# Optimization experiments

Hardware: AMD Instinct MI355X
Metric: run time of the kernel (lower is better)

The kernel has to match this reference:

```python
import jax, jax.numpy as jnp
import numpy as np

B, N, D, H = 2, 4096, 768, 12
HD = D // H  # head_dim = 64


def setup_inputs() -> dict:
    key = jax.random.key(0)
    k1, k2, k3, k4 = jax.random.split(key, 4)
    s = 1.0 / np.sqrt(D)
    return {
        "x": jax.random.normal(k1, (B, N, D), dtype=jnp.float32),
        "W_kqv": jax.random.normal(k2, (H, D, 3 * HD), dtype=jnp.float32) * s,
        "W_proj": jax.random.normal(k3, (D, D), dtype=jnp.float32) * s,
        "b_proj": jax.random.normal(k4, (D,), dtype=jnp.float32) * 0.02,
    }


def reference(x, W_kqv, W_proj, b_proj):
    # Per-head fused KQV projection: [B,N,D] x [H,D,3*HD] -> [B,H,N,3*HD]
    kqv = jnp.einsum("bnd,hde->bhne", x, W_kqv)
    # split order in source: k, q, v
    k, q, v = jnp.split(kqv, 3, axis=-1)  # each [B,H,N,HD]
    scale = 1.0 / np.sqrt(HD)
    scores = jnp.einsum("bhqd,bhkd->bhqk", q, k) * scale  # [B,H,N,N]
    causal = jnp.tril(jnp.ones((N, N), dtype=bool))
    scores = jnp.where(causal, scores, -jnp.inf)
    probs = jax.nn.softmax(scores, axis=-1)
    out = jnp.einsum("bhqk,bhkd->bhqd", probs, v)  # [B,H,N,HD]
    # concat heads along feature dim -> [B,N,D]
    out = out.transpose(0, 2, 1, 3).reshape(B, N, D)
    # output projection (dropout_rate=0.0 -> identity)
    return out @ W_proj.T + b_proj
```

## Files before the change

### kernel.cpp

```cpp
#include <hip/hip_runtime.h>

typedef _Float16 half8 __attribute__((ext_vector_type(8)));
typedef __fp16 fp16x2 __attribute__((ext_vector_type(2)));
typedef float floatx4 __attribute__((ext_vector_type(4)));
typedef float floatx16 __attribute__((ext_vector_type(16)));

#define MFMA_F16(a, b, c) __builtin_amdgcn_mfma_f32_16x16x32_f16((a), (b), (c), 0, 0, 0)
#define MFMA32(a, b, c) __builtin_amdgcn_mfma_f32_32x32x16_f16((a), (b), (c), 0, 0, 0)

__device__ __forceinline__ unsigned short f2h_bits(float f) {
    union { _Float16 h; unsigned short u; } cv;
    cv.h = (_Float16)f;
    return cv.u;
}

__device__ __forceinline__ float exp2_hw(float x) {
#if __has_builtin(__builtin_amdgcn_exp2f)
    return __builtin_amdgcn_exp2f(x);
#else
    return exp2f(x);
#endif
}

__device__ __forceinline__ unsigned pkrtz(float a, float b) {
    union { fp16x2 h; unsigned u; } cv;
    cv.h = __builtin_amdgcn_cvt_pkrtz(a, b);
    return cv.u;
}

__device__ __forceinline__ void swap32(unsigned a, unsigned b, int hi32,
                                       unsigned& r0, unsigned& r1) {
#if __has_builtin(__builtin_amdgcn_permlane32_swap)
    auto r = __builtin_amdgcn_permlane32_swap((int)a, (int)b, false, false);
    r0 = (unsigned)r[0];
    r1 = (unsigned)r[1];
#else
    unsigned ax = (unsigned)__shfl_xor((int)a, 32, 64);
    unsigned bx = (unsigned)__shfl_xor((int)b, 32, 64);
    r0 = hi32 ? bx : a;
    r1 = hi32 ? b : ax;
#endif
}

__device__ __forceinline__ float xhalf_max(float x) {
#if __has_builtin(__builtin_amdgcn_permlane32_swap)
    auto r = __builtin_amdgcn_permlane32_swap(__float_as_int(x), __float_as_int(x), false, false);
    return fmaxf(__int_as_float(r[0]), __int_as_float(r[1]));
#else
    return fmaxf(x, __shfl_xor(x, 32, 64));
#endif
}
__device__ __forceinline__ float xhalf_add(float x) {
#if __has_builtin(__builtin_amdgcn_permlane32_swap)
    auto r = __builtin_amdgcn_permlane32_swap(__float_as_int(x), __float_as_int(x), false, false);
    return __int_as_float(r[0]) + __int_as_float(r[1]);
#else
    return x + __shfl_xor(x, 32, 64);
#endif
}

__device__ __forceinline__ float bperm_f(int srclane, float v) {
    return __int_as_float(__builtin_amdgcn_ds_bpermute(srclane << 2, __float_as_int(v)));
}

__global__ void conv_x_kernel(const float* __restrict__ x, unsigned short* __restrict__ xb) {
    int i = blockIdx.x * 256 + threadIdx.x;
    float4 v = ((const float4*)x)[i];
    ushort4 o;
    o.x = f2h_bits(v.x); o.y = f2h_bits(v.y); o.z = f2h_bits(v.z); o.w = f2h_bits(v.w);
    ((ushort4*)xb)[i] = o;
}

__global__ void conv_wkqv_kernel(const float* __restrict__ w, unsigned short* __restrict__ wT) {
    int t = blockIdx.x * 256 + threadIdx.x;
    int d = t % 768;
    int hc = t / 768;
    int h = hc / 192;
    int c = hc - h * 192;
    float v = w[(h * 768 + d) * 192 + c];
    if (c >= 64 && c < 128) v *= 0.18033688011112042f;
    wT[t] = f2h_bits(v);
}

__global__ void conv_wproj_kernel(const float* __restrict__ w, unsigned short* __restrict__ wb) {
    int i = blockIdx.x * 256 + threadIdx.x;
    float4 v = ((const float4*)w)[i];
    ushort4 o;
    o.x = f2h_bits(v.x); o.y = f2h_bits(v.y); o.z = f2h_bits(v.z); o.w = f2h_bits(v.w);
    ((ushort4*)wb)[i] = o;
}

template <int EPI>
__global__ __launch_bounds__(256, 2) void gemm_bt_kernel(
    const unsigned short* __restrict__ A, const unsigned short* __restrict__ Bt,
    unsigned short* __restrict__ o_q, unsigned short* __restrict__ o_k,
    unsigned short* __restrict__ o_vt, float* __restrict__ o_f32,
    const float* __restrict__ bias, int Ntiles) {
    __shared__ unsigned short sA[128 * 64];
    __shared__ unsigned short sB[128 * 64];
    const int tid = threadIdx.x;
    const int lo = tid & 15;
    const int hi = (tid >> 4) & 3;
    const int wid = tid >> 6;
    const int wr = wid >> 1;
    const int wc = wid & 1;
    const int bm = blockIdx.x / Ntiles;
    const int bn = blockIdx.x % Ntiles;
    const size_t rowA0 = (size_t)bm * 128;
    const size_t rowB0 = (size_t)bn * 128;

    const floatx4 ZERO = {0.f, 0.f, 0.f, 0.f};
    floatx4 acc[4][4];
#pragma unroll
    for (int i = 0; i < 4; ++i)
#pragma unroll
        for (int j = 0; j < 4; ++j) acc[i][j] = ZERO;

    const int ldsWaveBase = (tid & 0xC0) << 3;

    for (int kt = 0; kt < 768; kt += 64) {
        __syncthreads();
#pragma unroll
        for (int it = 0; it < 4; ++it) {
            int g = it * 256 + tid;
            int row = g >> 3;
            int slot = g & 7;
            int koff = kt + ((slot ^ (row & 7)) << 3);
            const unsigned short* srcA = A + (rowA0 + row) * 768 + koff;
            const unsigned short* srcB = Bt + (rowB0 + row) * 768 + koff;
            unsigned short* dA = &sA[it * 2048 + ldsWaveBase];
            unsigned short* dB = &sB[it * 2048 + ldsWaveBase];
            __builtin_amdgcn_global_load_lds(
                (const __attribute__((address_space(1))) unsigned int*)srcA,
                (__attribute__((address_space(3))) unsigned int*)dA, 16, 0, 0);
            __builtin_amdgcn_global_load_lds(
                (const __attribute__((address_space(1))) unsigned int*)srcB,
                (__attribute__((address_space(3))) unsigned int*)dB, 16, 0, 0);
        }
        __syncthreads();
#pragma unroll
        for (int kc = 0; kc < 2; ++kc) {
            half8 av[4], bv[4];
#pragma unroll
            for (int mi = 0; mi < 4; ++mi) {
                int row = wr * 64 + mi * 16 + lo;
                av[mi] = *(const half8*)&sA[row * 64 + (((kc * 4 + hi) ^ (lo & 7)) << 3)];
            }
#pragma unroll
            for (int ni = 0; ni < 4; ++ni) {
                int row = wc * 64 + ni * 16 + lo;
                bv[ni] = *(const half8*)&sB[row * 64 + (((kc * 4 + hi) ^ (lo & 7)) << 3)];
            }
#pragma unroll
            for (int mi = 0; mi < 4; ++mi)
#pragma unroll
                for (int ni = 0; ni < 4; ++ni)
                    acc[mi][ni] = MFMA_F16(av[mi], bv[ni], acc[mi][ni]);
        }
    }

    if (EPI == 0) {
#pragma unroll
        for (int ni = 0; ni < 4; ++ni) {
            int gn = (int)rowB0 + wc * 64 + ni * 16 + lo;
            unsigned h = (unsigned)gn / 192u;
            int c = gn - (int)h * 192;
#pragma unroll
            for (int mi = 0; mi < 4; ++mi) {
#pragma unroll
                for (int r = 0; r < 4; ++r) {
                    int gm = (int)rowA0 + wr * 64 + mi * 16 + hi * 4 + r;
                    int b = gm >> 12;
                    int n = gm & 4095;
                    int bh = b * 12 + (int)h;
                    unsigned short val = f2h_bits(acc[mi][ni][r]);
                    if (c < 64) {
                        int t = n >> 5;
                        size_t idx = ((((size_t)bh * 128 + t) * 4 + (c >> 4)) * 64 +
                                      (((c >> 3) & 1) * 32 + (n & 31))) * 8 + (c & 7);
                        o_k[idx] = val;
                    } else if (c < 128) {
                        int d = c - 64;
                        int t = n >> 5;
                        size_t idx = ((((size_t)bh * 128 + t) * 4 + (d >> 4)) * 64 +
                                      (((d >> 3) & 1) * 32 + (n & 31))) * 8 + (d & 7);
                        o_q[idx] = val;
                    } else {
                        int dv = c - 128;
                        int t = n >> 5;
                        int kin = n & 31;
                        size_t idx = ((((size_t)bh * 128 + t) * 4 +
                                       ((dv >> 5) * 2 + (kin >> 4))) * 64 +
                                      (((kin >> 3) & 1) * 32 + (dv & 31))) * 8 + (kin & 7);
                        o_vt[idx] = val;
                    }
                }
            }
        }
    } else {
#pragma unroll
        for (int mi = 0; mi < 4; ++mi)
#pragma unroll
            for (int ni = 0; ni < 4; ++ni) {
                int gn = (int)rowB0 + wc * 64 + ni * 16 + lo;
                float bs = bias[gn];
#pragma unroll
                for (int r = 0; r < 4; ++r) {
                    int gm = (int)rowA0 + wr * 64 + mi * 16 + hi * 4 + r;
                    o_f32[(size_t)gm * 768 + gn] = acc[mi][ni][r] + bs;
                }
            }
    }
}

__global__ __launch_bounds__(128, 3) void attn_kernel(
    const unsigned short* __restrict__ Qw, const unsigned short* __restrict__ Kw,
    const unsigned short* __restrict__ Vtw, unsigned short* __restrict__ Ow) {
    __shared__ float sM[64 * 35];
    const int tid = threadIdx.x;
    const int lane = tid & 63;
    const int wid = tid >> 6;
    const int l31 = lane & 31;
    const int hi32 = lane >> 5;
    const int bh = blockIdx.x % 24;
    const int band = 127 - blockIdx.x / 24;
    const int b = bh / 12;
    const int h = bh - b * 12;

    const unsigned short* QF = Qw + (size_t)bh * 262144;
    const unsigned short* KF = Kw + (size_t)bh * 262144;
    const unsigned short* VF = Vtw + (size_t)bh * 262144;

    const floatx16 Z16 = {0.f,0.f,0.f,0.f,0.f,0.f,0.f,0.f,0.f,0.f,0.f,0.f,0.f,0.f,0.f,0.f};

    const int q0 = band << 5;
    const int myq = q0 + l31;
    const int nk = (band >> 1) + 1;

    half8 qf[4];
#pragma unroll
    for (int ds = 0; ds < 4; ++ds)
        qf[ds] = *(const half8*)&QF[(((size_t)band * 4 + ds) * 64 + lane) * 8];

    floatx16 accO0 = Z16, accO1 = Z16;
    float mI = -1e30f, lI = 0.f;

    for (int i = wid; i < nk; i += 2) {
        const int kt = i << 6;
        const unsigned short* kb = &KF[(size_t)(2 * i) * 2048 + lane * 8];
        half8 kfa[4], kfb[4];
#pragma unroll
        for (int ds = 0; ds < 4; ++ds) {
            kfa[ds] = *(const half8*)(kb + ds * 512);
            kfb[ds] = *(const half8*)(kb + 2048 + ds * 512);
        }
        const unsigned short* vb0 = &VF[(size_t)(2 * i) * 2048 + lane * 8];
        half8 vf0[2][2], vf1[2][2];
#pragma unroll
        for (int dt = 0; dt < 2; ++dt)
#pragma unroll
            for (int j = 0; j < 2; ++j) {
                vf0[dt][j] = *(const half8*)(vb0 + (dt * 2 + j) * 512);
                vf1[dt][j] = *(const half8*)(vb0 + 2048 + (dt * 2 + j) * 512);
            }

        floatx16 s0 = Z16, s1 = Z16;
        __builtin_amdgcn_s_setprio(1);
#pragma unroll
        for (int ds = 0; ds < 4; ++ds) s0 = MFMA32(kfa[ds], qf[ds], s0);
#pragma unroll
        for (int ds = 0; ds < 4; ++ds) s1 = MFMA32(kfb[ds], qf[ds], s1);
        __builtin_amdgcn_s_setprio(0);

        if (i == nk - 1) {
#pragma unroll
            for (int r = 0; r < 16; ++r) {
                int crow = (r & 3) + ((r >> 2) << 3) + (hi32 << 2);
                if (kt + crow > myq) s0[r] = -1e30f;
                if (kt + 32 + crow > myq) s1[r] = -1e30f;
            }
        }

        float ma[8];
#pragma unroll
        for (int r = 0; r < 8; ++r)
            ma[r] = fmaxf(fmaxf(s0[2 * r], s0[2 * r + 1]),
                          fmaxf(s1[2 * r], s1[2 * r + 1]));
        float mx = fmaxf(fmaxf(fmaxf(ma[0], ma[1]), fmaxf(ma[2], ma[3])),
                         fmaxf(fmaxf(ma[4], ma[5]), fmaxf(ma[6], ma[7])));
        mx = xhalf_max(mx);

        if (!__all(mx <= mI + 8.0f)) {
            float mn = fmaxf(mI, mx);
            float sc = exp2_hw(mI - mn);
            mI = mn;
            lI *= sc;
#pragma unroll
            for (int r = 0; r < 16; ++r) {
                int src = (r & 3) + ((r >> 2) << 3) + (hi32 << 2);
                float scb = bperm_f(src, sc);
                accO0[r] *= scb;
                accO1[r] *= scb;
            }
        }

#pragma unroll
        for (int r = 0; r < 16; ++r) {
            s0[r] = exp2_hw(s0[r] - mI);
            s1[r] = exp2_hw(s1[r] - mI);
        }
        float sa[8];
#pragma unroll
        for (int r = 0; r < 8; ++r)
            sa[r] = (s0[2 * r] + s0[2 * r + 1]) + (s1[2 * r] + s1[2 * r + 1]);
        float ps = ((sa[0] + sa[1]) + (sa[2] + sa[3])) +
                   ((sa[4] + sa[5]) + (sa[6] + sa[7]));
        lI += xhalf_add(ps);

        {
            unsigned pA0 = pkrtz(s0[0], s0[1]),   pA1 = pkrtz(s0[2], s0[3]);
            unsigned pB0 = pkrtz(s0[4], s0[5]),   pB1 = pkrtz(s0[6], s0[7]);
            unsigned pC0 = pkrtz(s0[8], s0[9]),   pC1 = pkrtz(s0[10], s0[11]);
            unsigned pD0 = pkrtz(s0[12], s0[13]), pD1 = pkrtz(s0[14], s0[15]);
            unsigned w0, w1, w2, w3, u0, u1, u2, u3;
            swap32(pA0, pB0, hi32, w0, w2);
            swap32(pA1, pB1, hi32, w1, w3);
            swap32(pC0, pD0, hi32, u0, u2);
            swap32(pC1, pD1, hi32, u1, u3);
            union { unsigned u[4]; half8 h; } f0, f1;
            f0.u[0] = w0; f0.u[1] = w1; f0.u[2] = w2; f0.u[3] = w3;
            f1.u[0] = u0; f1.u[1] = u1; f1.u[2] = u2; f1.u[3] = u3;
            __builtin_amdgcn_s_setprio(1);
            accO0 = MFMA32(f0.h, vf0[0][0], accO0);
            accO0 = MFMA32(f1.h, vf0[0][1], accO0);
            accO1 = MFMA32(f0.h, vf0[1][0], accO1);
            accO1 = MFMA32(f1.h, vf0[1][1], accO1);
            __builtin_amdgcn_s_setprio(0);
        }
        {
            unsigned pA0 = pkrtz(s1[0], s1[1]),   pA1 = pkrtz(s1[2], s1[3]);
            unsigned pB0 = pkrtz(s1[4], s1[5]),   pB1 = pkrtz(s1[6], s1[7]);
            unsigned pC0 = pkrtz(s1[8], s1[9]),   pC1 = pkrtz(s1[10], s1[11]);
            unsigned pD0 = pkrtz(s1[12], s1[13]), pD1 = pkrtz(s1[14], s1[15]);
            unsigned w0, w1, w2, w3, u0, u1, u2, u3;
            swap32(pA0, pB0, hi32, w0, w2);
            swap32(pA1, pB1, hi32, w1, w3);
            swap32(pC0, pD0, hi32, u0, u2);
            swap32(pC1, pD1, hi32, u1, u3);
            union { unsigned u[4]; half8 h; } f0, f1;
            f0.u[0] = w0; f0.u[1] = w1; f0.u[2] = w2; f0.u[3] = w3;
            f1.u[0] = u0; f1.u[1] = u1; f1.u[2] = u2; f1.u[3] = u3;
            __builtin_amdgcn_s_setprio(1);
            accO0 = MFMA32(f0.h, vf1[0][0], accO0);
            accO0 = MFMA32(f1.h, vf1[0][1], accO0);
            accO1 = MFMA32(f0.h, vf1[1][0], accO1);
            accO1 = MFMA32(f1.h, vf1[1][1], accO1);
            __builtin_amdgcn_s_setprio(0);
        }
    }

    if (wid == 1) {
        float* dst = &sM[lane * 35];
        dst[0] = mI;
        dst[1] = lI;
#pragma unroll
        for (int r = 0; r < 16; ++r) { dst[2 + r] = accO0[r]; dst[18 + r] = accO1[r]; }
    }
    __syncthreads();
    if (wid == 0) {
        const float* src = &sM[lane * 35];
        float m1 = src[0], l1 = src[1];
        float mstar = fmaxf(mI, m1);
        float sc0 = exp2_hw(mI - mstar);
        float sc1 = exp2_hw(m1 - mstar);
        float lt = lI * sc0 + l1 * sc1;
        float inv = 1.0f / lt;
        float f0 = sc0 * inv, f1 = sc1 * inv;
#pragma unroll
        for (int r = 0; r < 16; ++r) {
            int crow = (r & 3) + ((r >> 2) << 3) + (hi32 << 2);
            float fb0 = bperm_f(crow, f0);
            float fb1 = bperm_f(crow, f1);
            float o0 = accO0[r] * fb0 + src[2 + r] * fb1;
            float o1 = accO1[r] * fb0 + src[18 + r] * fb1;
            int qrow = q0 + crow;
            size_t base = ((size_t)(b * 4096 + qrow)) * 768 + h * 64;
            Ow[base + l31] = f2h_bits(o0);
            Ow[base + 32 + l31] = f2h_bits(o1);
        }
    }
}

extern "C" void kernel_launch(void* const* d_in, const int* in_sizes, int n_in,
                              void* d_out, int out_size, void* d_ws, size_t ws_size,
                              hipStream_t stream) {
    const float* x = (const float*)d_in[0];
    const float* wkqv = (const float*)d_in[1];
    const float* wproj = (const float*)d_in[2];
    const float* bproj = (const float*)d_in[3];
    float* out = (float*)d_out;

    char* ws = (char*)d_ws;
    unsigned short* xb = (unsigned short*)(ws);
    unsigned short* wkqvT = (unsigned short*)(ws + 12582912);
    unsigned short* wprojB = (unsigned short*)(ws + 16121856);
    unsigned short* Qw = (unsigned short*)(ws + 17301504);
    unsigned short* Kw = (unsigned short*)(ws + 29884416);
    unsigned short* Vtw = (unsigned short*)(ws + 42467328);
    unsigned short* Ow = xb;
    if (ws_size < 55050240) return;

    conv_x_kernel<<<6144, 256, 0, stream>>>(x, xb);
    conv_wkqv_kernel<<<6912, 256, 0, stream>>>(wkqv, wkqvT);
    conv_wproj_kernel<<<576, 256, 0, stream>>>(wproj, wprojB);
    gemm_bt_kernel<0><<<64 * 18, 256, 0, stream>>>(xb, wkqvT, Qw, Kw, Vtw, nullptr, nullptr, 18);
    attn_kernel<<<24 * 128, 128, 0, stream>>>(Qw, Kw, Vtw, Ow);
    gemm_bt_kernel<1><<<64 * 6, 256, 0, stream>>>(Ow, wprojB, nullptr, nullptr, nullptr, out, bproj, 6);
}
```

Before: 162.9 us.

## Share K tiles across two query bands via double-buffered LDS in attention

Attention blocks now own two adjacent 32-row query bands, one per wave, instead of splitting one band's key range across the two waves. Each key tile is loaded once into double-buffered LDS with async global-to-LDS loads and read by both waves, which removes the cross-wave softmax merge through shared memory and halves the grid. In exchange the blocks add two barriers per key step, have half as many blocks to spread across the GPU, and each wave walks the full key range serially. V is still read directly from global memory by each wave.

```diff
diff --git a/kernel.cpp b/kernel.cpp
--- a/kernel.cpp
+++ b/kernel.cpp
@@ -216,14 +216,15 @@
 __global__ __launch_bounds__(128, 3) void attn_kernel(
     const unsigned short* __restrict__ Qw, const unsigned short* __restrict__ Kw,
     const unsigned short* __restrict__ Vtw, unsigned short* __restrict__ Ow) {
-    __shared__ float sM[64 * 35];
+    __shared__ unsigned short sK[2][4096];
     const int tid = threadIdx.x;
     const int lane = tid & 63;
     const int wid = tid >> 6;
     const int l31 = lane & 31;
     const int hi32 = lane >> 5;
     const int bh = blockIdx.x % 24;
-    const int band = 127 - blockIdx.x / 24;
+    const int p = 63 - blockIdx.x / 24;
+    const int band = 2 * p + wid;
     const int b = bh / 12;
     const int h = bh - b * 12;
 
@@ -235,7 +236,7 @@
 
     const int q0 = band << 5;
     const int myq = q0 + l31;
-    const int nk = (band >> 1) + 1;
+    const int nk = p + 1;
 
     half8 qf[4];
 #pragma unroll
@@ -245,15 +246,36 @@
     floatx16 accO0 = Z16, accO1 = Z16;
     float mI = -1e30f, lI = 0.f;
 
-    for (int i = wid; i < nk; i += 2) {
+#pragma unroll
+    for (int j = 0; j < 4; ++j) {
+        int sl = wid * 4 + j;
+        const unsigned short* src = KF + sl * 512 + lane * 8;
+        unsigned short* dst = &sK[0][sl * 512];
+        __builtin_amdgcn_global_load_lds(
+            (const __attribute__((address_space(1))) unsigned int*)src,
+            (__attribute__((address_space(3))) unsigned int*)dst, 16, 0, 0);
+    }
+
+    int cur = 0;
+    for (int i = 0; i < nk; ++i) {
         const int kt = i << 6;
-        const unsigned short* kb = &KF[(size_t)(2 * i) * 2048 + lane * 8];
-        half8 kfa[4], kfb[4];
-#pragma unroll
-        for (int ds = 0; ds < 4; ++ds) {
-            kfa[ds] = *(const half8*)(kb + ds * 512);
-            kfb[ds] = *(const half8*)(kb + 2048 + ds * 512);
-        }
+        const bool more = (i + 1 < nk);
+        if (more) {
+#pragma unroll
+            for (int j = 0; j < 4; ++j) {
+                int sl = wid * 4 + j;
+                const unsigned short* src = KF + (size_t)(i + 1) * 4096 + sl * 512 + lane * 8;
+                unsigned short* dst = &sK[cur ^ 1][sl * 512];
+                __builtin_amdgcn_global_load_lds(
+                    (const __attribute__((address_space(1))) unsigned int*)src,
+                    (__attribute__((address_space(3))) unsigned int*)dst, 16, 0, 0);
+            }
+            asm volatile("s_waitcnt vmcnt(4)" ::: "memory");
+        } else {
+            asm volatile("s_waitcnt vmcnt(0)" ::: "memory");
+        }
+        __syncthreads();
+
         const unsigned short* vb0 = &VF[(size_t)(2 * i) * 2048 + lane * 8];
         half8 vf0[2][2], vf1[2][2];
 #pragma unroll
@@ -263,6 +285,14 @@
                 vf0[dt][j] = *(const half8*)(vb0 + (dt * 2 + j) * 512);
                 vf1[dt][j] = *(const half8*)(vb0 + 2048 + (dt * 2 + j) * 512);
             }
+
+        const unsigned short* kb = &sK[cur][0];
+        half8 kfa[4], kfb[4];
+#pragma unroll
+        for (int ds = 0; ds < 4; ++ds) {
+            kfa[ds] = *(const half8*)&kb[ds * 512 + lane * 8];
+            kfb[ds] = *(const half8*)&kb[2048 + ds * 512 + lane * 8];
+        }
 
         floatx16 s0 = Z16, s1 = Z16;
         __builtin_amdgcn_s_setprio(1);
@@ -357,37 +387,20 @@
             accO1 = MFMA32(f1.h, vf1[1][1], accO1);
             __builtin_amdgcn_s_setprio(0);
         }
+
+        __syncthreads();
+        cur ^= 1;
     }
 
-    if (wid == 1) {
-        float* dst = &sM[lane * 35];
-        dst[0] = mI;
-        dst[1] = lI;
-#pragma unroll
-        for (int r = 0; r < 16; ++r) { dst[2 + r] = accO0[r]; dst[18 + r] = accO1[r]; }
-    }
-    __syncthreads();
-    if (wid == 0) {
-        const float* src = &sM[lane * 35];
-        float m1 = src[0], l1 = src[1];
-        float mstar = fmaxf(mI, m1);
-        float sc0 = exp2_hw(mI - mstar);
-        float sc1 = exp2_hw(m1 - mstar);
-        float lt = lI * sc0 + l1 * sc1;
-        float inv = 1.0f / lt;
-        float f0 = sc0 * inv, f1 = sc1 * inv;
-#pragma unroll
-        for (int r = 0; r < 16; ++r) {
-            int crow = (r & 3) + ((r >> 2) << 3) + (hi32 << 2);
-            float fb0 = bperm_f(crow, f0);
-            float fb1 = bperm_f(crow, f1);
-            float o0 = accO0[r] * fb0 + src[2 + r] * fb1;
-            float o1 = accO1[r] * fb0 + src[18 + r] * fb1;
-            int qrow = q0 + crow;
-            size_t base = ((size_t)(b * 4096 + qrow)) * 768 + h * 64;
-            Ow[base + l31] = f2h_bits(o0);
-            Ow[base + 32 + l31] = f2h_bits(o1);
-        }
+    const float linv = 1.0f / lI;
+#pragma unroll
+    for (int r = 0; r < 16; ++r) {
+        int crow = (r & 3) + ((r >> 2) << 3) + (hi32 << 2);
+        float lb = bperm_f(crow, linv);
+        int qrow = q0 + crow;
+        size_t base = ((size_t)(b * 4096 + qrow)) * 768 + h * 64;
+        Ow[base + l31] = f2h_bits(accO0[r] * lb);
+        Ow[base + 32 + l31] = f2h_bits(accO1[r] * lb);
     }
 }
 
@@ -414,6 +427,6 @@
     conv_wkqv_kernel<<<6912, 256, 0, stream>>>(wkqv, wkqvT);
     conv_wproj_kernel<<<576, 256, 0, stream>>>(wproj, wprojB);
     gemm_bt_kernel<0><<<64 * 18, 256, 0, stream>>>(xb, wkqvT, Qw, Kw, Vtw, nullptr, nullptr, 18);
-    attn_kernel<<<24 * 128, 128, 0, stream>>>(Qw, Kw, Vtw, Ow);
+    attn_kernel<<<24 * 64, 128, 0, stream>>>(Qw, Kw, Vtw, Ow);
     gemm_bt_kernel<1><<<64 * 6, 256, 0, stream>>>(Ow, wprojB, nullptr, nullptr, nullptr, out, bproj, 6);
 }
```

New measurement: 183.6 us. +12.7%, slower.
